# Kernel tuning notes

Hardware: AMD Instinct MI355X
Metric: run time of the kernel (lower is better)

Reference implementation:

```python
import jax, jax.numpy as jnp
import numpy as np

B = 64        # number of tasks (sequential steps)
D = 512       # knowledge_representation_dim == understanding_representation_dim
M = 8192      # memory_slots
GAMMA = 0.95  # memory_gamma


def setup_inputs() -> dict:
    key = jax.random.key(0)
    k1, k2, k3, k4 = jax.random.split(key, 4)
    ortho = jax.nn.initializers.orthogonal()
    return {
        "k": jax.random.normal(k1, (B, 1, D), jnp.float32),
        "u": jax.random.normal(k2, (B, 1, D), jnp.float32),
        "memory_knowledge": ortho(k3, (D, M), jnp.float32),
        "memory_understanding": ortho(k4, (D, M), jnp.float32),
        "beta_param": jnp.float32(0.0),
        "memory_gamma": jnp.float32(GAMMA),
    }


def reference(k, u, memory_knowledge, memory_understanding, beta_param, memory_gamma):
    n_slots = memory_knowledge.shape[1]
    slot_ids = jnp.arange(n_slots)
    beta = jax.nn.sigmoid(beta_param)

    def step(carry, xs):
        MK, MU, w_w, w_u, w_lu = carry
        k_task, u_task = xs  # each [1, D]
        # cosine similarity of the task key against every memory column: [1, M]
        sim = (k_task @ MK) / (
            jnp.linalg.norm(k_task, axis=-1, keepdims=True)
            * jnp.linalg.norm(MK, axis=0, keepdims=True)
        )
        w_r = jax.nn.softmax(sim, axis=-1)[0]  # [M]
        # zero out the least-used slot (argmin of usage weights)
        keep = (slot_ids != jnp.argmin(w_u))[None, :]  # [1, M]
        MK = jnp.where(keep, MK, 0.0)
        MU = jnp.where(keep, MU, 0.0)
        # usage / write / least-used weight updates
        w_u = memory_gamma * w_u + w_r + w_w
        w_w = beta * jnp.mean(w_r) + (1.0 - beta) * w_lu  # [M] via broadcast of scalar mean
        w_lu = (slot_ids == jnp.argmin(w_u)).astype(MK.dtype)  # one-hot least-used
        # rank-1 write of understanding, then read refined understanding, then write knowledge
        MU = MU + u_task[0][:, None] * w_w[None, :]  # [D, M]
        u_ref = w_r @ MK.T  # [D] -- read uses MK after zeroing, before its write
        MK = MK + k_task[0][:, None] * w_w[None, :]  # [D, M]
        return (MK, MU, w_w, w_u, w_lu), u_ref

    zeros = jnp.zeros((n_slots,), memory_knowledge.dtype)
    init = (memory_knowledge, memory_understanding, zeros, zeros, zeros)
    _, u_refined = jax.lax.scan(step, init, (k, u))
    return u_refined[:, None, :]  # [B, 1, D]
```

## Files before the change

kernel.cpp:

```cpp
#include <hip/hip_runtime.h>
#include <math.h>

#define BB 64
#define DD 512
#define MM 8192
#define K2T 512
#define K2C 16

typedef unsigned long long u64;

template<int CTRL>
__device__ __forceinline__ float dpp_addf(float x) {
    int y = __builtin_amdgcn_update_dpp(0, __float_as_int(x), CTRL, 0xF, 0xF, true);
    return x + __int_as_float(y);
}
__device__ __forceinline__ float wave_sum64(float x) {
    x = dpp_addf<0x111>(x); x = dpp_addf<0x112>(x); x = dpp_addf<0x114>(x); x = dpp_addf<0x118>(x);
    x = dpp_addf<0x142>(x); x = dpp_addf<0x143>(x);
    return __int_as_float(__builtin_amdgcn_readlane(__float_as_int(x), 63));
}
__device__ __forceinline__ float readlane_f(float v, int l) {
    return __int_as_float(__builtin_amdgcn_readlane(__float_as_int(v), l));
}
template<int CTRL>
__device__ __forceinline__ u64 dpp_min_step(u64 k) {
    unsigned lo = (unsigned)k, hi = (unsigned)(k >> 32);
    unsigned nlo = (unsigned)__builtin_amdgcn_update_dpp((int)0xFFFFFFFFu, (int)lo, CTRL, 0xF, 0xF, false);
    unsigned nhi = (unsigned)__builtin_amdgcn_update_dpp((int)0xFFFFFFFFu, (int)hi, CTRL, 0xF, 0xF, false);
    u64 nk = (((u64)nhi) << 32) | (u64)nlo;
    return nk < k ? nk : k;
}
__device__ __forceinline__ u64 wave_min64_lane63(u64 k) {
    k = dpp_min_step<0x111>(k); k = dpp_min_step<0x112>(k); k = dpp_min_step<0x114>(k);
    k = dpp_min_step<0x118>(k); k = dpp_min_step<0x142>(k); k = dpp_min_step<0x143>(k);
    return k;
}
__device__ __forceinline__ u64 wave_min8(u64 k) {
    k = dpp_min_step<0x111>(k); k = dpp_min_step<0x112>(k); k = dpp_min_step<0x114>(k);
    unsigned lo = (unsigned)__builtin_amdgcn_readlane((int)(unsigned)k, 7);
    unsigned hi = (unsigned)__builtin_amdgcn_readlane((int)(unsigned)(k >> 32), 7);
    return (((u64)hi) << 32) | (u64)lo;
}

struct K0Smem {
    float Ks[BB][129];
    float Gs[BB][BB];
};
struct K1Smem {
    float Ks[64 * 65];
    float Ms[64 * 65];
    float sq[4 * 64];
};
#define KA_SMEM ((sizeof(K0Smem) > sizeof(K1Smem)) ? sizeof(K0Smem) : sizeof(K1Smem))

__global__ __launch_bounds__(256) void ka_gram_s0(const float* __restrict__ K, const float* __restrict__ MK0,
                                                  float* __restrict__ G, float* __restrict__ Pfx,
                                                  float* __restrict__ S0p, float* __restrict__ n2p) {
    __shared__ __align__(16) char blob[KA_SMEM];
    const int tid = threadIdx.x;

    if (blockIdx.x == 0) {
        K0Smem* sm = (K0Smem*)blob;
        const int ti = ((tid >> 4) & 15) << 2;
        const int tj = (tid & 15) << 2;
        float acc[4][4];
        #pragma unroll
        for (int i = 0; i < 4; ++i)
            #pragma unroll
            for (int j = 0; j < 4; ++j) acc[i][j] = 0.f;
        for (int d0 = 0; d0 < DD; d0 += 128) {
            #pragma unroll
            for (int i = 0; i < 32; ++i) {
                int e = i * 256 + tid; int r = e >> 7, c = e & 127;
                sm->Ks[r][c] = K[r * DD + d0 + c];
            }
            __syncthreads();
            for (int dl = 0; dl < 128; ++dl) {
                float rv[4], cv[4];
                #pragma unroll
                for (int i = 0; i < 4; ++i) rv[i] = sm->Ks[ti + i][dl];
                #pragma unroll
                for (int j = 0; j < 4; ++j) cv[j] = sm->Ks[tj + j][dl];
                #pragma unroll
                for (int i = 0; i < 4; ++i)
                    #pragma unroll
                    for (int j = 0; j < 4; ++j) acc[i][j] += rv[i] * cv[j];
            }
            __syncthreads();
        }
        #pragma unroll
        for (int i = 0; i < 4; ++i)
            #pragma unroll
            for (int j = 0; j < 4; ++j) {
                G[(ti + i) * BB + tj + j] = acc[i][j];
                sm->Gs[ti + i][tj + j] = acc[i][j];
            }
        __syncthreads();
        const int s = tid & 63, w = tid >> 6;
        for (int rr = 0; rr < 16; ++rr) {
            int row = w * 16 + rr;
            float x = (s < row) ? sm->Gs[row][s] : 0.f;
            #pragma unroll
            for (int o = 1; o < 64; o <<= 1) {
                float y = __shfl_down(x, o);
                if (s + o < 64) x += y;
            }
            Pfx[row * BB + s] = x;
        }
        return;
    }

    K1Smem* sm = (K1Smem*)blob;
    const int b = blockIdx.x - 1;
    const int lane = tid & 63, w = tid >> 6;
    const int jb = (b & 127) * 64;
    const int by = b >> 7;
    const int dbase = by * 256;
    const int t4 = ((w << 2) | (lane >> 4)) << 2;
    const int jq0 = lane & 15;
    float acc[4][4];
    #pragma unroll
    for (int i = 0; i < 4; ++i)
        #pragma unroll
        for (int q = 0; q < 4; ++q) acc[i][q] = 0.f;
    float sqa = 0.f;
    for (int dt = 0; dt < 4; ++dt) {
        int d0 = dbase + dt * 64;
        #pragma unroll
        for (int i = 0; i < 16; ++i) {
            int e = i * 256 + tid; int r = e >> 6, c = e & 63;
            sm->Ks[r * 65 + c] = K[r * DD + d0 + c];
            float m = MK0[(d0 + r) * MM + jb + c];
            sm->Ms[r * 65 + c] = m;
            sqa += m * m;
        }
        __syncthreads();
        #pragma unroll 4
        for (int dl = 0; dl < 64; ++dl) {
            float kv[4], mv[4];
            #pragma unroll
            for (int i = 0; i < 4; ++i) kv[i] = sm->Ks[(t4 + i) * 65 + dl];
            #pragma unroll
            for (int q = 0; q < 4; ++q) mv[q] = sm->Ms[dl * 65 + jq0 + 16 * q];
            #pragma unroll
            for (int i = 0; i < 4; ++i)
                #pragma unroll
                for (int q = 0; q < 4; ++q) acc[i][q] += kv[i] * mv[q];
        }
        __syncthreads();
    }
    #pragma unroll
    for (int i = 0; i < 4; ++i)
        #pragma unroll
        for (int q = 0; q < 4; ++q)
            S0p[by * BB * MM + (t4 + i) * MM + jb + jq0 + 16 * q] = acc[i][q];
    sm->sq[w * 64 + lane] = sqa;
    __syncthreads();
    if (w == 0) n2p[by * MM + jb + lane] =
        sm->sq[lane] + sm->sq[64 + lane] + sm->sq[128 + lane] + sm->sq[192 + lane];
}

__global__ __launch_bounds__(64) void k1b_ecold(const float* __restrict__ S0p,
                                                const float* __restrict__ G,
                                                const float* __restrict__ Pfx,
                                                const float* __restrict__ n2p,
                                                const float* __restrict__ bp,
                                                float* __restrict__ Ecold) {
    __shared__ float Pfx0s[BB], invks[BB], k2s[BB];
    int tid = threadIdx.x;
    int j = blockIdx.x * 64 + tid;
    {
        float g = G[tid * BB + tid];
        k2s[tid] = g;
        invks[tid] = __builtin_amdgcn_rsqf(g);
        Pfx0s[tid] = Pfx[tid * BB + 0];
    }
    const float beta = 1.f / (1.f + expf(-bp[0]));
    const float cuni = beta / (float)MM;
    float n2c = n2p[j] + n2p[MM + j];
    __syncthreads();
    float pa = S0p[j];
    float pb = S0p[BB * MM + j];
    for (int t = 0; t < BB; ++t) {
        float na = 0.f, nb = 0.f;
        if (t + 1 < BB) {
            na = S0p[(t + 1) * MM + j];
            nb = S0p[(BB + t + 1) * MM + j];
        }
        float s0 = pa + pb;
        float d_ = s0 + cuni * Pfx0s[t];
        float cosv = d_ * invks[t] * __builtin_amdgcn_rsqf(n2c);
        float ee = __expf(cosv);
        Ecold[t * MM + j] = ee;
        n2c = n2c + 2.f * cuni * d_ + cuni * cuni * k2s[t];
        pa = na; pb = nb;
    }
}

__global__ __launch_bounds__(256) void ks_rowsum(const float* __restrict__ Ecold, float* __restrict__ Scold) {
    __shared__ float sw[4];
    int t = blockIdx.x, tid = threadIdx.x;
    int lane = tid & 63, wid = tid >> 6;
    float s = 0.f;
    #pragma unroll
    for (int i = 0; i < 32; ++i) s += Ecold[t * MM + i * 256 + tid];
    #pragma unroll
    for (int o = 32; o > 0; o >>= 1) s += __shfl_down(s, o);
    if (lane == 0) sw[wid] = s;
    __syncthreads();
    if (tid == 0) Scold[t] = sw[0] + sw[1] + sw[2] + sw[3];
}

struct ScanSmem {
    u64   red[2][8];
    float EtabL[BB * BB];
    float EcTabL[BB * BB];
    float invSL[BB];
    float SL[BB];
    int   endL[BB];
    float invS_bc[2];
};
struct K3Smem {
    float Ws[64 * 65];
    float Msub[64 * 65];
};
#define SMEM_BYTES ((sizeof(ScanSmem) > sizeof(K3Smem)) ? sizeof(ScanSmem) : sizeof(K3Smem))

__global__ __launch_bounds__(512) void k23_scan_u1(const float* __restrict__ Ecold,
                                                   const float* __restrict__ G,
                                                   const float* __restrict__ Pfx,
                                                   const float* __restrict__ Scoldg,
                                                   const float* __restrict__ bp,
                                                   const float* __restrict__ gp,
                                                   const float* __restrict__ MK0,
                                                   float* __restrict__ Etab_g,
                                                   float* __restrict__ EcTab_g,
                                                   float* __restrict__ Sg,
                                                   float* __restrict__ invSg,
                                                   int*   __restrict__ endTab_g,
                                                   int*   __restrict__ hcolg,
                                                   float* __restrict__ parts) {
    __shared__ __align__(16) char smem_raw[SMEM_BYTES];
    const int tid = threadIdx.x;

    if (blockIdx.x != 0) {
        K3Smem* sm = (K3Smem*)smem_raw;
        const int tile = blockIdx.x - 1;
        const int d0 = (tile & 7) * 64;
        const int by = tile >> 3;
        const bool act = tid < 256;
        const int lane = tid & 63, w = tid >> 6;
        const int t4 = ((w << 2) | (lane >> 4)) << 2;
        const int dq0 = lane & 15;
        float acc[4][4];
        #pragma unroll
        for (int i = 0; i < 4; ++i)
            #pragma unroll
            for (int q = 0; q < 4; ++q) acc[i][q] = 0.f;
        for (int sub = 0; sub < 4; ++sub) {
            int jb = by * 256 + sub * 64;
            if (act) {
                #pragma unroll
                for (int i = 0; i < 16; ++i) {
                    int e = i * 256 + tid; int r = e >> 6, c = e & 63;
                    sm->Ws[r * 65 + c] = Ecold[r * MM + jb + c];
                    sm->Msub[r * 65 + c] = MK0[(d0 + r) * MM + jb + c];
                }
            }
            __syncthreads();
            if (act) {
                #pragma unroll 4
                for (int jl = 0; jl < 64; ++jl) {
                    float wv[4], mv[4];
                    #pragma unroll
                    for (int i = 0; i < 4; ++i) wv[i] = sm->Ws[(t4 + i) * 65 + jl];
                    #pragma unroll
                    for (int q = 0; q < 4; ++q) mv[q] = sm->Msub[(dq0 + 16 * q) * 65 + jl];
                    #pragma unroll
                    for (int i = 0; i < 4; ++i)
                        #pragma unroll
                        for (int q = 0; q < 4; ++q) acc[i][q] += wv[i] * mv[q];
                }
            }
            __syncthreads();
        }
        if (act) {
            #pragma unroll
            for (int i = 0; i < 4; ++i)
                #pragma unroll
                for (int q = 0; q < 4; ++q)
                    parts[(by * 64 + t4 + i) * DD + d0 + dq0 + 16 * q] = acc[i][q];
        }
        return;
    }

    ScanSmem* sm = (ScanSmem*)smem_raw;
    const int lane = tid & 63;
    const int wid = tid >> 6;
    const bool w0 = (wid == 0);

    const float beta  = 1.f / (1.f + expf(-bp[0]));
    const float gamma = gp[0];
    const float cuni  = beta / (float)MM;
    const float omb   = 1.f - beta;

    if (tid < BB) sm->endL[tid] = BB;

    const float4* Ec4 = reinterpret_cast<const float4*>(Ecold);

    float wu[K2C], e0[K2C], e1[K2C], e2[K2C];
    #pragma unroll
    for (int c = 0; c < K2C; ++c) wu[c] = 0.f;
    #pragma unroll
    for (int i = 0; i < K2C / 4; ++i) {
        float4 v = Ec4[i * K2T + tid];
        e0[4 * i + 0] = v.x; e0[4 * i + 1] = v.y; e0[4 * i + 2] = v.z; e0[4 * i + 3] = v.w;
        float4 u = Ec4[(MM / 4) + i * K2T + tid];
        e1[4 * i + 0] = u.x; e1[4 * i + 1] = u.y; e1[4 * i + 2] = u.z; e1[4 * i + 3] = u.w;
    }

    float slot_n2 = 0.f, slot_ec = 0.f, wu_hot = 0.f, e_true_c = 0.f;
    int   slot_j = -1;
    bool  slot_act = false;
    float k2_cur = 0.f, S_reg = 0.f, invS_reg = 0.f;

    if (w0) {
        float g0 = G[lane];
        k2_cur = readlane_f(g0, 0);
        S_reg = Scoldg[0];
        invS_reg = __builtin_amdgcn_rcpf(S_reg);
        if (lane == 0) sm->invS_bc[0] = invS_reg;
    }
    __syncthreads();

    auto step = [&](int t, float (&cur)[K2C], float (&ld)[K2C]) {
        float grow_n = 0.f, pfx_n = 0.f, Ssc_n = 0.f, ecpf0 = 0.f;
        if (w0 && t + 1 < BB) {
            if (slot_act) ecpf0 = Ecold[(t + 1) * MM + slot_j];
            grow_n = G[(t + 1) * BB + lane];
            pfx_n  = Pfx[(t + 1) * BB + lane];
            Ssc_n  = Scoldg[t + 1];
        }

        int j0; float minval;
        if (t == 0) { j0 = 0; minval = 0.f; }
        else {
            u64 pm = sm->red[t & 1][lane & 7];
            pm = wave_min8(pm);
            j0 = (int)(pm & 0xFFFFFFFFu);
            minval = __uint_as_float((unsigned)(pm >> 32));
        }
        const float cuni_t = (t == 0) ? 0.f : cuni;
        float invS = w0 ? invS_reg : sm->invS_bc[t & 1];

        float latev = 0.f, ecpf_t = 0.f;
        if (w0 && lane == t) {
            latev = Ecold[t * MM + j0];
            if (t + 1 < BB) ecpf_t = Ecold[(t + 1) * MM + j0];
        }
        __builtin_amdgcn_sched_barrier(0);
        if (t + 2 < BB) {
            #pragma unroll
            for (int i = 0; i < K2C / 4; ++i) {
                float4 v = Ec4[(t + 2) * (MM / 4) + i * K2T + tid];
                ld[4 * i + 0] = v.x; ld[4 * i + 1] = v.y; ld[4 * i + 2] = v.z; ld[4 * i + 3] = v.w;
            }
        }
        __builtin_amdgcn_sched_barrier(0);

        bool fresh = false;
        if (w0) {
            u64 sup = __ballot(slot_act && (slot_j == j0));
            const bool has_sup = (sup != 0ull);
            const int  ssup = has_sup ? (int)__builtin_ctzll(sup) : 0;

            if (slot_act) {
                float ww = cuni + ((t >= 2 && lane == t - 1) ? omb : 0.f);
                wu_hot = fmaf(gamma, wu_hot, fmaf(e_true_c, invS, ww));
            }
            float trans_wu = readlane_f(wu_hot, ssup);
            float trans_E  = readlane_f(e_true_c, ssup);

            if (lane == t) {
                slot_j = j0;
                float ww0 = cuni + ((t >= 1) ? omb : 0.f);
                slot_n2 = ww0 * ww0 * k2_cur;
                slot_act = true;
                if (has_sup) wu_hot = trans_wu;
                fresh = !has_sup;
            }
            if (has_sup) {
                if (lane == ssup) slot_act = false;
                if (lane == t) sm->endL[ssup] = t;
            }

            float etl = e_true_c, ecl = slot_ec;
            if (lane == t) { ecl = latev; etl = has_sup ? trans_E : latev; }
            sm->EtabL[t * BB + lane]  = etl;
            sm->EcTabL[t * BB + lane] = ecl;
            if (lane == 0) { sm->invSL[t] = invS; sm->SL[t] = S_reg; }

            if (fresh) wu_hot = fmaf(gamma, minval, fmaf(latev, invS, cuni_t));

            if (t + 1 < BB) {
                float d_ = cuni * pfx_n;
                if (lane >= 1) d_ += omb * grow_n;
                float k2n   = readlane_f(grow_n, t + 1);
                float invkn = __builtin_amdgcn_rsqf(k2n);
                float ecpf  = (lane == t) ? ecpf_t : ecpf0;
                float myDelta = 0.f;
                float e_n = 0.f;
                if (slot_act) {
                    e_n = __expf(d_ * invkn * __builtin_amdgcn_rsqf(slot_n2));
                    myDelta = e_n - ecpf;
                    slot_n2 = slot_n2 + 2.f * cuni * d_ + cuni * cuni * k2n;
                }
                float S_next = Ssc_n + wave_sum64(myDelta);
                float invS_next = __builtin_amdgcn_rcpf(S_next);
                if (lane == 0) sm->invS_bc[(t + 1) & 1] = invS_next;
                if (slot_act) slot_ec = ecpf;
                e_true_c = e_n;
                k2_cur = k2n;
                S_reg = S_next; invS_reg = invS_next;
            }
        }

        float vmin = 0.f; int jmin = 0;
        #pragma unroll
        for (int i = 0; i < 4; ++i) {
            #pragma unroll
            for (int q = 0; q < 4; ++q) {
                int c = i * 4 + q;
                float wun = fmaf(gamma, wu[c], fmaf(cur[c], invS, cuni_t));
                wu[c] = wun;
                int j = i * 2048 + (tid << 2) + q;
                if (c == 0) { vmin = wun; jmin = j; }
                else if (wun < vmin) { vmin = wun; jmin = j; }
            }
        }
        u64 key = (((u64)__float_as_uint(vmin)) << 32) | (unsigned)jmin;

        if (((j0 >> 2) & (K2T - 1)) == tid) {
            int cj = ((j0 >> 11) << 2) | (j0 & 3);
            #pragma unroll
            for (int c = 0; c < K2C; ++c) if (c == cj) wu[c] = __builtin_inff();
        }

        if (w0) {
            u64 skey = (slot_act && !fresh)
                     ? ((((u64)__float_as_uint(wu_hot)) << 32) | (unsigned)slot_j) : ~0ull;
            key = skey < key ? skey : key;
        }
        key = wave_min64_lane63(key);
        if (lane == 63) sm->red[(t + 1) & 1][wid] = key;

        asm volatile("s_waitcnt lgkmcnt(0)" ::: "memory");
        __builtin_amdgcn_s_barrier();
        asm volatile("" ::: "memory");
    };

    #pragma unroll 1
    for (int th = 0; th < 63; th += 3) {
        step(th + 0, e0, e2);
        step(th + 1, e1, e0);
        step(th + 2, e2, e1);
    }
    step(63, e0, e2);

    for (int i = tid; i < BB * BB; i += K2T) {
        Etab_g[i]  = sm->EtabL[i];
        EcTab_g[i] = sm->EcTabL[i];
    }
    if (tid < BB) {
        Sg[tid] = sm->SL[tid];
        invSg[tid] = sm->invSL[tid];
        endTab_g[tid] = sm->endL[tid];
    }
    if (w0) hcolg[lane] = slot_j;
}

__global__ __launch_bounds__(512) void k3b_gather(const float* __restrict__ MK0, const int* __restrict__ hcolg,
                                                  float* __restrict__ MKhot) {
    int i = blockIdx.x, d = threadIdx.x;
    int h = hcolg[i];
    MKhot[i * DD + d] = MK0[d * MM + h];
}

__global__ __launch_bounds__(512) void k4_final(const float* __restrict__ parts,
                                                const float* __restrict__ K,
                                                const float* __restrict__ Etab,
                                                const float* __restrict__ EcTab,
                                                const int*   __restrict__ endTab,
                                                const float* __restrict__ Sg,
                                                const float* __restrict__ invSg,
                                                const float* __restrict__ MKhot,
                                                const float* __restrict__ bp,
                                                float* __restrict__ out) {
    __shared__ float Arow[BB];
    __shared__ float Drow[BB];
    int t = blockIdx.x, d = threadIdx.x;
    if (d < BB) {
        const float beta = 1.f / (1.f + expf(-bp[0]));
        const float cuni = beta / (float)MM;
        const float omb  = 1.f - beta;
        int s = d;
        float Ev = Etab[t * BB + s];
        int endv = endTab[s];
        bool act = (s <= t) && (t < endv);
        float S = Sg[t], invS = invSg[t];
        float ev = act ? Ev : 0.f;
        float x = ev;
        #pragma unroll
        for (int o = 1; o < 64; o <<= 1) {
            float y = __shfl_down(x, o);
            if (s + o < 64) x += y;
        }
        float suf = x - ev;
        float arow = 0.f;
        if (s < t) {
            float Qe = S - suf;
            arow = cuni * Qe;
            if (s >= 1 && act) arow += omb * Ev;
            arow *= invS;
        }
        Arow[s] = arow;
        Drow[s] = act ? (-invS * EcTab[t * BB + s]) : 0.f;
    }
    __syncthreads();
    float isv = invSg[t];
    float s1 = 0.f;
    #pragma unroll
    for (int p = 0; p < 32; ++p) s1 += parts[(p * 64 + t) * DD + d];
    float s2 = 0.f;
    for (int i = 0; i < BB; ++i) s2 += Drow[i] * MKhot[i * DD + d];
    float s3 = 0.f;
    for (int i = 0; i < BB; ++i) s3 += Arow[i] * K[i * DD + d];
    out[t * DD + d] = isv * s1 + s2 + s3;
}

extern "C" void kernel_launch(void* const* d_in, const int* in_sizes, int n_in,
                              void* d_out, int out_size, void* d_ws, size_t ws_size,
                              hipStream_t stream) {
    const float* K   = (const float*)d_in[0];
    const float* MK0 = (const float*)d_in[2];
    const float* bp  = (const float*)d_in[4];
    const float* gp  = (const float*)d_in[5];

    float* ws    = (float*)d_ws;
    float* G     = ws;
    float* Pfx   = G + 4096;
    float* S0p   = Pfx + 4096;
    float* n2p   = S0p + 1048576;
    float* Ecold = n2p + 16384;
    float* Scold = Ecold + 524288;
    float* Etab  = Scold + 64;
    float* EcTab = Etab + 4096;
    float* Sarr  = EcTab + 4096;
    float* invS  = Sarr + 64;
    float* MKhot = invS + 64;
    float* parts = MKhot + 32768;
    int*   hcol  = (int*)(parts + 1048576);
    int*   endT  = hcol + 64;
    float* out   = (float*)d_out;

    ka_gram_s0  <<<257, 256, 0, stream>>>(K, MK0, G, Pfx, S0p, n2p);
    k1b_ecold   <<<128, 64, 0, stream>>>(S0p, G, Pfx, n2p, bp, Ecold);
    ks_rowsum   <<<64, 256, 0, stream>>>(Ecold, Scold);
    k23_scan_u1 <<<257, 512, 0, stream>>>(Ecold, G, Pfx, Scold, bp, gp, MK0,
                                          Etab, EcTab, Sarr, invS, endT, hcol, parts);
    k3b_gather  <<<64, 512, 0, stream>>>(MK0, hcol, MKhot);
    k4_final    <<<64, 512, 0, stream>>>(parts, K, Etab, EcTab, endT, Sarr, invS, MKhot, bp, out);
}
```

Before: 214.6 us.

## Fuse six kernels into two using in-kernel flag synchronization

Merges the Gram/S0 kernel with the Ecold and rowsum kernels: each block now covers the full D range for its 64 columns, keeps S0 in shared memory and emits per-block partial row sums. The final output kernel and the hot-column gather move into the scan kernel as extra blocks that spin on atomic flags until the scan and partial-product tiles are done. This removes several launches and the S0p/n2p/MKhot round trips through global memory. In exchange there are fewer blocks (129 versus 257) in the first kernel, spin-waits that rely on co-residency of all blocks, and a memset launch.

After: 257.8 us. 20.1% more time.

```diff
diff --git a/kernel.cpp b/kernel.cpp
--- a/kernel.cpp
+++ b/kernel.cpp
@@ -42,21 +42,38 @@
     return (((u64)hi) << 32) | (u64)lo;
 }
 
+__device__ __forceinline__ void flag_release(int* p, int v) {
+    __threadfence();
+    __hip_atomic_store(p, v, __ATOMIC_RELEASE, __HIP_MEMORY_SCOPE_AGENT);
+}
+__device__ __forceinline__ void spin_until_eq(int* p, int want) {
+    while (__hip_atomic_load(p, __ATOMIC_ACQUIRE, __HIP_MEMORY_SCOPE_AGENT) != want)
+        __builtin_amdgcn_s_sleep(2);
+}
+
 struct K0Smem {
     float Ks[BB][129];
     float Gs[BB][BB];
 };
-struct K1Smem {
+struct KbSmem {
     float Ks[64 * 65];
     float Ms[64 * 65];
+    float S0s[64 * 65];
     float sq[4 * 64];
+    float n2A[64];
+    float n2full[64];
+    float Pfx0s[BB], invks[BB], k2s[BB];
 };
-#define KA_SMEM ((sizeof(K0Smem) > sizeof(K1Smem)) ? sizeof(K0Smem) : sizeof(K1Smem))
-
-__global__ __launch_bounds__(256) void ka_gram_s0(const float* __restrict__ K, const float* __restrict__ MK0,
-                                                  float* __restrict__ G, float* __restrict__ Pfx,
-                                                  float* __restrict__ S0p, float* __restrict__ n2p) {
-    __shared__ __align__(16) char blob[KA_SMEM];
+#define KAB_SMEM ((sizeof(K0Smem) > sizeof(KbSmem)) ? sizeof(K0Smem) : sizeof(KbSmem))
+
+__global__ __launch_bounds__(256) void kab_gram_ecold(const float* __restrict__ K,
+                                                      const float* __restrict__ MK0,
+                                                      const float* __restrict__ bp,
+                                                      float* __restrict__ G, float* __restrict__ Pfx,
+                                                      float* __restrict__ Ecold,
+                                                      float* __restrict__ Spart,
+                                                      int* __restrict__ flags) {
+    __shared__ __align__(16) char blob[KAB_SMEM];
     const int tid = threadIdx.x;
 
     if (blockIdx.x == 0) {
@@ -107,32 +124,33 @@
             }
             Pfx[row * BB + s] = x;
         }
+        __syncthreads();
+        if (tid == 0) flag_release(&flags[0], 1);
         return;
     }
 
-    K1Smem* sm = (K1Smem*)blob;
+    KbSmem* sm = (KbSmem*)blob;
     const int b = blockIdx.x - 1;
     const int lane = tid & 63, w = tid >> 6;
-    const int jb = (b & 127) * 64;
-    const int by = b >> 7;
-    const int dbase = by * 256;
+    const int jb = b * 64;
     const int t4 = ((w << 2) | (lane >> 4)) << 2;
     const int jq0 = lane & 15;
-    float acc[4][4];
+
+    float accA[4][4], accB[4][4];
     #pragma unroll
     for (int i = 0; i < 4; ++i)
         #pragma unroll
-        for (int q = 0; q < 4; ++q) acc[i][q] = 0.f;
-    float sqa = 0.f;
+        for (int q = 0; q < 4; ++q) { accA[i][q] = 0.f; accB[i][q] = 0.f; }
+    float sqaA = 0.f, sqaB = 0.f;
     for (int dt = 0; dt < 4; ++dt) {
-        int d0 = dbase + dt * 64;
+        int d0 = dt * 64;
         #pragma unroll
         for (int i = 0; i < 16; ++i) {
             int e = i * 256 + tid; int r = e >> 6, c = e & 63;
             sm->Ks[r * 65 + c] = K[r * DD + d0 + c];
             float m = MK0[(d0 + r) * MM + jb + c];
             sm->Ms[r * 65 + c] = m;
-            sqa += m * m;
+            sqaA += m * m;
         }
         __syncthreads();
         #pragma unroll 4
@@ -145,70 +163,75 @@
             #pragma unroll
             for (int i = 0; i < 4; ++i)
                 #pragma unroll
-                for (int q = 0; q < 4; ++q) acc[i][q] += kv[i] * mv[q];
-        }
-        __syncthreads();
+                for (int q = 0; q < 4; ++q) accA[i][q] += kv[i] * mv[q];
+        }
+        __syncthreads();
+    }
+    for (int dt = 0; dt < 4; ++dt) {
+        int d0 = 256 + dt * 64;
+        #pragma unroll
+        for (int i = 0; i < 16; ++i) {
+            int e = i * 256 + tid; int r = e >> 6, c = e & 63;
+            sm->Ks[r * 65 + c] = K[r * DD + d0 + c];
+            float m = MK0[(d0 + r) * MM + jb + c];
+            sm->Ms[r * 65 + c] = m;
+            sqaB += m * m;
+        }
+        __syncthreads();
+        #pragma unroll 4
+        for (int dl = 0; dl < 64; ++dl) {
+            float kv[4], mv[4];
+            #pragma unroll
+            for (int i = 0; i < 4; ++i) kv[i] = sm->Ks[(t4 + i) * 65 + dl];
+            #pragma unroll
+            for (int q = 0; q < 4; ++q) mv[q] = sm->Ms[dl * 65 + jq0 + 16 * q];
+            #pragma unroll
+            for (int i = 0; i < 4; ++i)
+                #pragma unroll
+                for (int q = 0; q < 4; ++q) accB[i][q] += kv[i] * mv[q];
+        }
+        __syncthreads();
+    }
+    sm->sq[w * 64 + lane] = sqaA;
+    __syncthreads();
+    if (w == 0) sm->n2A[lane] = sm->sq[lane] + sm->sq[64 + lane] + sm->sq[128 + lane] + sm->sq[192 + lane];
+    __syncthreads();
+    sm->sq[w * 64 + lane] = sqaB;
+    __syncthreads();
+    if (w == 0) {
+        float b4 = sm->sq[lane] + sm->sq[64 + lane] + sm->sq[128 + lane] + sm->sq[192 + lane];
+        sm->n2full[lane] = sm->n2A[lane] + b4;
     }
     #pragma unroll
     for (int i = 0; i < 4; ++i)
         #pragma unroll
         for (int q = 0; q < 4; ++q)
-            S0p[by * BB * MM + (t4 + i) * MM + jb + jq0 + 16 * q] = acc[i][q];
-    sm->sq[w * 64 + lane] = sqa;
+            sm->S0s[(t4 + i) * 65 + jq0 + 16 * q] = accA[i][q] + accB[i][q];
+    if (tid == 0) spin_until_eq(&flags[0], 1);
     __syncthreads();
-    if (w == 0) n2p[by * MM + jb + lane] =
-        sm->sq[lane] + sm->sq[64 + lane] + sm->sq[128 + lane] + sm->sq[192 + lane];
-}
-
-__global__ __launch_bounds__(64) void k1b_ecold(const float* __restrict__ S0p,
-                                                const float* __restrict__ G,
-                                                const float* __restrict__ Pfx,
-                                                const float* __restrict__ n2p,
-                                                const float* __restrict__ bp,
-                                                float* __restrict__ Ecold) {
-    __shared__ float Pfx0s[BB], invks[BB], k2s[BB];
-    int tid = threadIdx.x;
-    int j = blockIdx.x * 64 + tid;
-    {
+    if (tid < BB) {
         float g = G[tid * BB + tid];
-        k2s[tid] = g;
-        invks[tid] = __builtin_amdgcn_rsqf(g);
-        Pfx0s[tid] = Pfx[tid * BB + 0];
-    }
-    const float beta = 1.f / (1.f + expf(-bp[0]));
-    const float cuni = beta / (float)MM;
-    float n2c = n2p[j] + n2p[MM + j];
+        sm->k2s[tid] = g;
+        sm->invks[tid] = __builtin_amdgcn_rsqf(g);
+        sm->Pfx0s[tid] = Pfx[tid * BB + 0];
+    }
     __syncthreads();
-    float pa = S0p[j];
-    float pb = S0p[BB * MM + j];
-    for (int t = 0; t < BB; ++t) {
-        float na = 0.f, nb = 0.f;
-        if (t + 1 < BB) {
-            na = S0p[(t + 1) * MM + j];
-            nb = S0p[(BB + t + 1) * MM + j];
-        }
-        float s0 = pa + pb;
-        float d_ = s0 + cuni * Pfx0s[t];
-        float cosv = d_ * invks[t] * __builtin_amdgcn_rsqf(n2c);
-        float ee = __expf(cosv);
-        Ecold[t * MM + j] = ee;
-        n2c = n2c + 2.f * cuni * d_ + cuni * cuni * k2s[t];
-        pa = na; pb = nb;
-    }
-}
-
-__global__ __launch_bounds__(256) void ks_rowsum(const float* __restrict__ Ecold, float* __restrict__ Scold) {
-    __shared__ float sw[4];
-    int t = blockIdx.x, tid = threadIdx.x;
-    int lane = tid & 63, wid = tid >> 6;
-    float s = 0.f;
-    #pragma unroll
-    for (int i = 0; i < 32; ++i) s += Ecold[t * MM + i * 256 + tid];
-    #pragma unroll
-    for (int o = 32; o > 0; o >>= 1) s += __shfl_down(s, o);
-    if (lane == 0) sw[wid] = s;
-    __syncthreads();
-    if (tid == 0) Scold[t] = sw[0] + sw[1] + sw[2] + sw[3];
+    if (w == 0) {
+        const float beta = 1.f / (1.f + expf(-bp[0]));
+        const float cuni = beta / (float)MM;
+        int j = jb + lane;
+        float n2c = sm->n2full[lane];
+        for (int t = 0; t < BB; ++t) {
+            float s0 = sm->S0s[t * 65 + lane];
+            float d_ = s0 + cuni * sm->Pfx0s[t];
+            float cosv = d_ * sm->invks[t] * __builtin_amdgcn_rsqf(n2c);
+            float ee = __expf(cosv);
+            Ecold[t * MM + j] = ee;
+            float rs = wave_sum64(ee);
+            if (lane == 0) Spart[t * 128 + b] = rs;
+            n2c = n2c + 2.f * cuni * d_ + cuni * cuni * sm->k2s[t];
+        }
+    }
 }
 
 struct ScanSmem {
@@ -224,28 +247,38 @@
     float Ws[64 * 65];
     float Msub[64 * 65];
 };
-#define SMEM_BYTES ((sizeof(ScanSmem) > sizeof(K3Smem)) ? sizeof(ScanSmem) : sizeof(K3Smem))
-
-__global__ __launch_bounds__(512) void k23_scan_u1(const float* __restrict__ Ecold,
-                                                   const float* __restrict__ G,
-                                                   const float* __restrict__ Pfx,
-                                                   const float* __restrict__ Scoldg,
-                                                   const float* __restrict__ bp,
-                                                   const float* __restrict__ gp,
-                                                   const float* __restrict__ MK0,
-                                                   float* __restrict__ Etab_g,
-                                                   float* __restrict__ EcTab_g,
-                                                   float* __restrict__ Sg,
-                                                   float* __restrict__ invSg,
-                                                   int*   __restrict__ endTab_g,
-                                                   int*   __restrict__ hcolg,
-                                                   float* __restrict__ parts) {
+struct K4Smem {
+    float Arow[BB];
+    float Drow[BB];
+    int   hcs[BB];
+};
+#define SM3 ((sizeof(ScanSmem) > sizeof(K3Smem)) ? sizeof(ScanSmem) : sizeof(K3Smem))
+#define SMEM_BYTES ((SM3 > sizeof(K4Smem)) ? SM3 : sizeof(K4Smem))
+
+__global__ __launch_bounds__(512) void k23_mega(const float* __restrict__ Ecold,
+                                                const float* __restrict__ G,
+                                                const float* __restrict__ Pfx,
+                                                const float* __restrict__ Spart,
+                                                const float* __restrict__ bp,
+                                                const float* __restrict__ gp,
+                                                const float* __restrict__ MK0,
+                                                const float* __restrict__ K,
+                                                float* __restrict__ Etab_g,
+                                                float* __restrict__ EcTab_g,
+                                                float* __restrict__ Sg,
+                                                float* __restrict__ invSg,
+                                                int*   __restrict__ endTab_g,
+                                                int*   __restrict__ hcolg,
+                                                float* __restrict__ parts,
+                                                float* __restrict__ out,
+                                                int*   __restrict__ flags) {
     __shared__ __align__(16) char smem_raw[SMEM_BYTES];
     const int tid = threadIdx.x;
-
-    if (blockIdx.x != 0) {
+    const int bx = blockIdx.x;
+
+    if (bx >= 1 && bx <= 256) {
         K3Smem* sm = (K3Smem*)smem_raw;
-        const int tile = blockIdx.x - 1;
+        const int tile = bx - 1;
         const int d0 = (tile & 7) * 64;
         const int by = tile >> 3;
         const bool act = tid < 256;
@@ -291,6 +324,59 @@
                 for (int q = 0; q < 4; ++q)
                     parts[(by * 64 + t4 + i) * DD + d0 + dq0 + 16 * q] = acc[i][q];
         }
+        __syncthreads();
+        if (tid == 0) { __threadfence(); atomicAdd(&flags[2], 1); }
+        return;
+    }
+
+    if (bx >= 257) {
+        K4Smem* sm = (K4Smem*)smem_raw;
+        const int t = bx - 257;
+        const int d = tid;
+        if (tid == 0) {
+            spin_until_eq(&flags[1], 1);
+            while (__hip_atomic_load(&flags[2], __ATOMIC_ACQUIRE, __HIP_MEMORY_SCOPE_AGENT) < 256)
+                __builtin_amdgcn_s_sleep(2);
+        }
+        __syncthreads();
+        if (d < BB) {
+            sm->hcs[d] = hcolg[d];
+            const float beta = 1.f / (1.f + expf(-bp[0]));
+            const float cuni = beta / (float)MM;
+            const float omb  = 1.f - beta;
+            int s = d;
+            float Ev = Etab_g[t * BB + s];
+            int endv = endTab_g[s];
+            bool act = (s <= t) && (t < endv);
+            float S = Sg[t], invS = invSg[t];
+            float ev = act ? Ev : 0.f;
+            float x = ev;
+            #pragma unroll
+            for (int o = 1; o < 64; o <<= 1) {
+                float y = __shfl_down(x, o);
+                if (s + o < 64) x += y;
+            }
+            float suf = x - ev;
+            float arow = 0.f;
+            if (s < t) {
+                float Qe = S - suf;
+                arow = cuni * Qe;
+                if (s >= 1 && act) arow += omb * Ev;
+                arow *= invS;
+            }
+            sm->Arow[s] = arow;
+            sm->Drow[s] = act ? (-invS * EcTab_g[t * BB + s]) : 0.f;
+        }
+        __syncthreads();
+        float isv = invSg[t];
+        float s1 = 0.f;
+        #pragma unroll
+        for (int p = 0; p < 32; ++p) s1 += parts[(p * 64 + t) * DD + d];
+        float s2 = 0.f;
+        for (int i = 0; i < BB; ++i) s2 += sm->Drow[i] * MK0[d * MM + sm->hcs[i]];
+        float s3 = 0.f;
+        for (int i = 0; i < BB; ++i) s3 += sm->Arow[i] * K[i * DD + d];
+        out[t * DD + d] = isv * s1 + s2 + s3;
         return;
     }
 
@@ -319,6 +405,18 @@
         e1[4 * i + 0] = u.x; e1[4 * i + 1] = u.y; e1[4 * i + 2] = u.z; e1[4 * i + 3] = u.w;
     }
 
+    float scold_r = 0.f;
+    if (w0) {
+        const float4* sp4 = reinterpret_cast<const float4*>(Spart + lane * 128);
+        float sc = 0.f;
+        #pragma unroll 8
+        for (int i = 0; i < 32; ++i) {
+            float4 v = sp4[i];
+            sc += v.x; sc += v.y; sc += v.z; sc += v.w;
+        }
+        scold_r = sc;
+    }
+
     float slot_n2 = 0.f, slot_ec = 0.f, wu_hot = 0.f, e_true_c = 0.f;
     int   slot_j = -1;
     bool  slot_act = false;
@@ -327,7 +425,7 @@
     if (w0) {
         float g0 = G[lane];
         k2_cur = readlane_f(g0, 0);
-        S_reg = Scoldg[0];
+        S_reg = readlane_f(scold_r, 0);
         invS_reg = __builtin_amdgcn_rcpf(S_reg);
         if (lane == 0) sm->invS_bc[0] = invS_reg;
     }
@@ -339,7 +437,7 @@
             if (slot_act) ecpf0 = Ecold[(t + 1) * MM + slot_j];
             grow_n = G[(t + 1) * BB + lane];
             pfx_n  = Pfx[(t + 1) * BB + lane];
-            Ssc_n  = Scoldg[t + 1];
+            Ssc_n  = readlane_f(scold_r, t + 1);
         }
 
         int j0; float minval;
@@ -477,65 +575,8 @@
         endTab_g[tid] = sm->endL[tid];
     }
     if (w0) hcolg[lane] = slot_j;
-}
-
-__global__ __launch_bounds__(512) void k3b_gather(const float* __restrict__ MK0, const int* __restrict__ hcolg,
-                                                  float* __restrict__ MKhot) {
-    int i = blockIdx.x, d = threadIdx.x;
-    int h = hcolg[i];
-    MKhot[i * DD + d] = MK0[d * MM + h];
-}
-
-__global__ __launch_bounds__(512) void k4_final(const float* __restrict__ parts,
-                                                const float* __restrict__ K,
-                                                const float* __restrict__ Etab,
-                                                const float* __restrict__ EcTab,
-                                                const int*   __restrict__ endTab,
-                                                const float* __restrict__ Sg,
-                                                const float* __restrict__ invSg,
-                                                const float* __restrict__ MKhot,
-                                                const float* __restrict__ bp,
-                                                float* __restrict__ out) {
-    __shared__ float Arow[BB];
-    __shared__ float Drow[BB];
-    int t = blockIdx.x, d = threadIdx.x;
-    if (d < BB) {
-        const float beta = 1.f / (1.f + expf(-bp[0]));
-        const float cuni = beta / (float)MM;
-        const float omb  = 1.f - beta;
-        int s = d;
-        float Ev = Etab[t * BB + s];
-        int endv = endTab[s];
-        bool act = (s <= t) && (t < endv);
-        float S = Sg[t], invS = invSg[t];
-        float ev = act ? Ev : 0.f;
-        float x = ev;
-        #pragma unroll
-        for (int o = 1; o < 64; o <<= 1) {
-            float y = __shfl_down(x, o);
-            if (s + o < 64) x += y;
-        }
-        float suf = x - ev;
-        float arow = 0.f;
-        if (s < t) {
-            float Qe = S - suf;
-            arow = cuni * Qe;
-            if (s >= 1 && act) arow += omb * Ev;
-            arow *= invS;
-        }
-        Arow[s] = arow;
-        Drow[s] = act ? (-invS * EcTab[t * BB + s]) : 0.f;
-    }
     __syncthreads();
-    float isv = invSg[t];
-    float s1 = 0.f;
-    #pragma unroll
-    for (int p = 0; p < 32; ++p) s1 += parts[(p * 64 + t) * DD + d];
-    float s2 = 0.f;
-    for (int i = 0; i < BB; ++i) s2 += Drow[i] * MKhot[i * DD + d];
-    float s3 = 0.f;
-    for (int i = 0; i < BB; ++i) s3 += Arow[i] * K[i * DD + d];
-    out[t * DD + d] = isv * s1 + s2 + s3;
+    if (tid == 0) flag_release(&flags[1], 1);
 }
 
 extern "C" void kernel_launch(void* const* d_in, const int* in_sizes, int n_in,
@@ -549,25 +590,20 @@
     float* ws    = (float*)d_ws;
     float* G     = ws;
     float* Pfx   = G + 4096;
-    float* S0p   = Pfx + 4096;
-    float* n2p   = S0p + 1048576;
-    float* Ecold = n2p + 16384;
-    float* Scold = Ecold + 524288;
-    float* Etab  = Scold + 64;
+    float* Ecold = Pfx + 4096;
+    float* Spart = Ecold + 524288;
+    float* Etab  = Spart + 8192;
     float* EcTab = Etab + 4096;
     float* Sarr  = EcTab + 4096;
     float* invS  = Sarr + 64;
-    float* MKhot = invS + 64;
-    float* parts = MKhot + 32768;
+    float* parts = invS + 64;
     int*   hcol  = (int*)(parts + 1048576);
     int*   endT  = hcol + 64;
+    int*   flags = endT + 64;
     float* out   = (float*)d_out;
 
-    ka_gram_s0  <<<257, 256, 0, stream>>>(K, MK0, G, Pfx, S0p, n2p);
-    k1b_ecold   <<<128, 64, 0, stream>>>(S0p, G, Pfx, n2p, bp, Ecold);
-    ks_rowsum   <<<64, 256, 0, stream>>>(Ecold, Scold);
-    k23_scan_u1 <<<257, 512, 0, stream>>>(Ecold, G, Pfx, Scold, bp, gp, MK0,
-                                          Etab, EcTab, Sarr, invS, endT, hcol, parts);
-    k3b_gather  <<<64, 512, 0, stream>>>(MK0, hcol, MKhot);
-    k4_final    <<<64, 512, 0, stream>>>(parts, K, Etab, EcTab, endT, Sarr, invS, MKhot, bp, out);
-}
+    hipMemsetAsync(flags, 0, 3 * sizeof(int), stream);
+    kab_gram_ecold <<<129, 256, 0, stream>>>(K, MK0, bp, G, Pfx, Ecold, Spart, flags);
+    k23_mega       <<<321, 512, 0, stream>>>(Ecold, G, Pfx, Spart, bp, gp, MK0, K,
+                                             Etab, EcTab, Sarr, invS, endT, hcol, parts, out, flags);
+}
```

## Fuse row-sum into ecold and final combine into scan kernel via flags

Applied to the files above, without the earlier changes.

Folds the per-row exp sums into k1b_ecold as per-block wave partials, and drops the separate row-sum kernel. The scan block sums those partials itself. The gather and final kernels are merged into k23_scan_u1: blocks 1..64 spin on global flags until the scan block and all 256 tile blocks finish, then compute the output and read the hot columns directly from MK0. This removes three launches and an intermediate buffer, but relies on every block being co-resident and adds spin-wait overhead plus a memset launch.

After: 271.3 us. +26.4%, slower.

```diff
diff --git a/kernel.cpp b/kernel.cpp
--- a/kernel.cpp
+++ b/kernel.cpp
@@ -40,6 +40,15 @@
     unsigned lo = (unsigned)__builtin_amdgcn_readlane((int)(unsigned)k, 7);
     unsigned hi = (unsigned)__builtin_amdgcn_readlane((int)(unsigned)(k >> 32), 7);
     return (((u64)hi) << 32) | (u64)lo;
+}
+
+__device__ __forceinline__ void flag_release(int* p, int v) {
+    __threadfence();
+    __hip_atomic_store(p, v, __ATOMIC_RELEASE, __HIP_MEMORY_SCOPE_AGENT);
+}
+__device__ __forceinline__ void spin_until_eq(int* p, int want) {
+    while (__hip_atomic_load(p, __ATOMIC_ACQUIRE, __HIP_MEMORY_SCOPE_AGENT) != want)
+        __builtin_amdgcn_s_sleep(2);
 }
 
 struct K0Smem {
@@ -165,10 +174,12 @@
                                                 const float* __restrict__ Pfx,
                                                 const float* __restrict__ n2p,
                                                 const float* __restrict__ bp,
-                                                float* __restrict__ Ecold) {
+                                                float* __restrict__ Ecold,
+                                                float* __restrict__ Spart) {
     __shared__ float Pfx0s[BB], invks[BB], k2s[BB];
     int tid = threadIdx.x;
-    int j = blockIdx.x * 64 + tid;
+    const int b = blockIdx.x;
+    int j = b * 64 + tid;
     {
         float g = G[tid * BB + tid];
         k2s[tid] = g;
@@ -192,23 +203,11 @@
         float cosv = d_ * invks[t] * __builtin_amdgcn_rsqf(n2c);
         float ee = __expf(cosv);
         Ecold[t * MM + j] = ee;
+        float rs = wave_sum64(ee);
+        if (tid == 0) Spart[t * 128 + b] = rs;
         n2c = n2c + 2.f * cuni * d_ + cuni * cuni * k2s[t];
         pa = na; pb = nb;
     }
-}
-
-__global__ __launch_bounds__(256) void ks_rowsum(const float* __restrict__ Ecold, float* __restrict__ Scold) {
-    __shared__ float sw[4];
-    int t = blockIdx.x, tid = threadIdx.x;
-    int lane = tid & 63, wid = tid >> 6;
-    float s = 0.f;
-    #pragma unroll
-    for (int i = 0; i < 32; ++i) s += Ecold[t * MM + i * 256 + tid];
-    #pragma unroll
-    for (int o = 32; o > 0; o >>= 1) s += __shfl_down(s, o);
-    if (lane == 0) sw[wid] = s;
-    __syncthreads();
-    if (tid == 0) Scold[t] = sw[0] + sw[1] + sw[2] + sw[3];
 }
 
 struct ScanSmem {
@@ -224,73 +223,136 @@
     float Ws[64 * 65];
     float Msub[64 * 65];
 };
-#define SMEM_BYTES ((sizeof(ScanSmem) > sizeof(K3Smem)) ? sizeof(ScanSmem) : sizeof(K3Smem))
+struct K4Smem {
+    float Arow[BB];
+    float Drow[BB];
+    int   hcs[BB];
+};
+#define SM3 ((sizeof(ScanSmem) > sizeof(K3Smem)) ? sizeof(ScanSmem) : sizeof(K3Smem))
+#define SMEM_BYTES ((SM3 > sizeof(K4Smem)) ? SM3 : sizeof(K4Smem))
 
 __global__ __launch_bounds__(512) void k23_scan_u1(const float* __restrict__ Ecold,
                                                    const float* __restrict__ G,
                                                    const float* __restrict__ Pfx,
-                                                   const float* __restrict__ Scoldg,
+                                                   const float* __restrict__ Spart,
                                                    const float* __restrict__ bp,
                                                    const float* __restrict__ gp,
                                                    const float* __restrict__ MK0,
+                                                   const float* __restrict__ K,
                                                    float* __restrict__ Etab_g,
                                                    float* __restrict__ EcTab_g,
                                                    float* __restrict__ Sg,
                                                    float* __restrict__ invSg,
                                                    int*   __restrict__ endTab_g,
                                                    int*   __restrict__ hcolg,
-                                                   float* __restrict__ parts) {
+                                                   float* __restrict__ parts,
+                                                   float* __restrict__ out,
+                                                   int*   __restrict__ flags) {
     __shared__ __align__(16) char smem_raw[SMEM_BYTES];
     const int tid = threadIdx.x;
-
-    if (blockIdx.x != 0) {
-        K3Smem* sm = (K3Smem*)smem_raw;
-        const int tile = blockIdx.x - 1;
-        const int d0 = (tile & 7) * 64;
-        const int by = tile >> 3;
-        const bool act = tid < 256;
-        const int lane = tid & 63, w = tid >> 6;
-        const int t4 = ((w << 2) | (lane >> 4)) << 2;
-        const int dq0 = lane & 15;
-        float acc[4][4];
-        #pragma unroll
-        for (int i = 0; i < 4; ++i)
-            #pragma unroll
-            for (int q = 0; q < 4; ++q) acc[i][q] = 0.f;
-        for (int sub = 0; sub < 4; ++sub) {
-            int jb = by * 256 + sub * 64;
+    const int bx = blockIdx.x;
+
+    if (bx != 0) {
+        {
+            K3Smem* sm = (K3Smem*)smem_raw;
+            const int tile = bx - 1;
+            const int d0 = (tile & 7) * 64;
+            const int by = tile >> 3;
+            const bool act = tid < 256;
+            const int lane = tid & 63, w = tid >> 6;
+            const int t4 = ((w << 2) | (lane >> 4)) << 2;
+            const int dq0 = lane & 15;
+            float acc[4][4];
+            #pragma unroll
+            for (int i = 0; i < 4; ++i)
+                #pragma unroll
+                for (int q = 0; q < 4; ++q) acc[i][q] = 0.f;
+            for (int sub = 0; sub < 4; ++sub) {
+                int jb = by * 256 + sub * 64;
+                if (act) {
+                    #pragma unroll
+                    for (int i = 0; i < 16; ++i) {
+                        int e = i * 256 + tid; int r = e >> 6, c = e & 63;
+                        sm->Ws[r * 65 + c] = Ecold[r * MM + jb + c];
+                        sm->Msub[r * 65 + c] = MK0[(d0 + r) * MM + jb + c];
+                    }
+                }
+                __syncthreads();
+                if (act) {
+                    #pragma unroll 4
+                    for (int jl = 0; jl < 64; ++jl) {
+                        float wv[4], mv[4];
+                        #pragma unroll
+                        for (int i = 0; i < 4; ++i) wv[i] = sm->Ws[(t4 + i) * 65 + jl];
+                        #pragma unroll
+                        for (int q = 0; q < 4; ++q) mv[q] = sm->Msub[(dq0 + 16 * q) * 65 + jl];
+                        #pragma unroll
+                        for (int i = 0; i < 4; ++i)
+                            #pragma unroll
+                            for (int q = 0; q < 4; ++q) acc[i][q] += wv[i] * mv[q];
+                    }
+                }
+                __syncthreads();
+            }
             if (act) {
                 #pragma unroll
-                for (int i = 0; i < 16; ++i) {
-                    int e = i * 256 + tid; int r = e >> 6, c = e & 63;
-                    sm->Ws[r * 65 + c] = Ecold[r * MM + jb + c];
-                    sm->Msub[r * 65 + c] = MK0[(d0 + r) * MM + jb + c];
-                }
+                for (int i = 0; i < 4; ++i)
+                    #pragma unroll
+                    for (int q = 0; q < 4; ++q)
+                        parts[(by * 64 + t4 + i) * DD + d0 + dq0 + 16 * q] = acc[i][q];
             }
             __syncthreads();
-            if (act) {
-                #pragma unroll 4
-                for (int jl = 0; jl < 64; ++jl) {
-                    float wv[4], mv[4];
-                    #pragma unroll
-                    for (int i = 0; i < 4; ++i) wv[i] = sm->Ws[(t4 + i) * 65 + jl];
-                    #pragma unroll
-                    for (int q = 0; q < 4; ++q) mv[q] = sm->Msub[(dq0 + 16 * q) * 65 + jl];
-                    #pragma unroll
-                    for (int i = 0; i < 4; ++i)
-                        #pragma unroll
-                        for (int q = 0; q < 4; ++q) acc[i][q] += wv[i] * mv[q];
-                }
-            }
-            __syncthreads();
-        }
-        if (act) {
-            #pragma unroll
-            for (int i = 0; i < 4; ++i)
-                #pragma unroll
-                for (int q = 0; q < 4; ++q)
-                    parts[(by * 64 + t4 + i) * DD + d0 + dq0 + 16 * q] = acc[i][q];
-        }
+            if (tid == 0) { __threadfence(); atomicAdd(&flags[1], 1); }
+        }
+        if (bx > 64) return;
+
+        K4Smem* sm = (K4Smem*)smem_raw;
+        const int t = bx - 1;
+        const int d = tid;
+        if (tid == 0) {
+            spin_until_eq(&flags[0], 1);
+            while (__hip_atomic_load(&flags[1], __ATOMIC_ACQUIRE, __HIP_MEMORY_SCOPE_AGENT) < 256)
+                __builtin_amdgcn_s_sleep(2);
+        }
+        __syncthreads();
+        if (d < BB) {
+            sm->hcs[d] = hcolg[d];
+            const float beta = 1.f / (1.f + expf(-bp[0]));
+            const float cuni = beta / (float)MM;
+            const float omb  = 1.f - beta;
+            int s = d;
+            float Ev = Etab_g[t * BB + s];
+            int endv = endTab_g[s];
+            bool act = (s <= t) && (t < endv);
+            float S = Sg[t], invS = invSg[t];
+            float ev = act ? Ev : 0.f;
+            float x = ev;
+            #pragma unroll
+            for (int o = 1; o < 64; o <<= 1) {
+                float y = __shfl_down(x, o);
+                if (s + o < 64) x += y;
+            }
+            float suf = x - ev;
+            float arow = 0.f;
+            if (s < t) {
+                float Qe = S - suf;
+                arow = cuni * Qe;
+                if (s >= 1 && act) arow += omb * Ev;
+                arow *= invS;
+            }
+            sm->Arow[s] = arow;
+            sm->Drow[s] = act ? (-invS * EcTab_g[t * BB + s]) : 0.f;
+        }
+        __syncthreads();
+        float isv = invSg[t];
+        float s1 = 0.f;
+        #pragma unroll
+        for (int p = 0; p < 32; ++p) s1 += parts[(p * 64 + t) * DD + d];
+        float s2 = 0.f;
+        for (int i = 0; i < BB; ++i) s2 += sm->Drow[i] * MK0[d * MM + sm->hcs[i]];
+        float s3 = 0.f;
+        for (int i = 0; i < BB; ++i) s3 += sm->Arow[i] * K[i * DD + d];
+        out[t * DD + d] = isv * s1 + s2 + s3;
         return;
     }
 
@@ -319,6 +381,18 @@
         e1[4 * i + 0] = u.x; e1[4 * i + 1] = u.y; e1[4 * i + 2] = u.z; e1[4 * i + 3] = u.w;
     }
 
+    float scold_r = 0.f;
+    if (w0) {
+        const float4* sp4 = reinterpret_cast<const float4*>(Spart + lane * 128);
+        float sc = 0.f;
+        #pragma unroll 8
+        for (int i = 0; i < 32; ++i) {
+            float4 v = sp4[i];
+            sc += v.x; sc += v.y; sc += v.z; sc += v.w;
+        }
+        scold_r = sc;
+    }
+
     float slot_n2 = 0.f, slot_ec = 0.f, wu_hot = 0.f, e_true_c = 0.f;
     int   slot_j = -1;
     bool  slot_act = false;
@@ -327,7 +401,7 @@
     if (w0) {
         float g0 = G[lane];
         k2_cur = readlane_f(g0, 0);
-        S_reg = Scoldg[0];
+        S_reg = readlane_f(scold_r, 0);
         invS_reg = __builtin_amdgcn_rcpf(S_reg);
         if (lane == 0) sm->invS_bc[0] = invS_reg;
     }
@@ -339,7 +413,7 @@
             if (slot_act) ecpf0 = Ecold[(t + 1) * MM + slot_j];
             grow_n = G[(t + 1) * BB + lane];
             pfx_n  = Pfx[(t + 1) * BB + lane];
-            Ssc_n  = Scoldg[t + 1];
+            Ssc_n  = readlane_f(scold_r, t + 1);
         }
 
         int j0; float minval;
@@ -477,65 +551,8 @@
         endTab_g[tid] = sm->endL[tid];
     }
     if (w0) hcolg[lane] = slot_j;
-}
-
-__global__ __launch_bounds__(512) void k3b_gather(const float* __restrict__ MK0, const int* __restrict__ hcolg,
-                                                  float* __restrict__ MKhot) {
-    int i = blockIdx.x, d = threadIdx.x;
-    int h = hcolg[i];
-    MKhot[i * DD + d] = MK0[d * MM + h];
-}
-
-__global__ __launch_bounds__(512) void k4_final(const float* __restrict__ parts,
-                                                const float* __restrict__ K,
-                                                const float* __restrict__ Etab,
-                                                const float* __restrict__ EcTab,
-                                                const int*   __restrict__ endTab,
-                                                const float* __restrict__ Sg,
-                                                const float* __restrict__ invSg,
-                                                const float* __restrict__ MKhot,
-                                                const float* __restrict__ bp,
-                                                float* __restrict__ out) {
-    __shared__ float Arow[BB];
-    __shared__ float Drow[BB];
-    int t = blockIdx.x, d = threadIdx.x;
-    if (d < BB) {
-        const float beta = 1.f / (1.f + expf(-bp[0]));
-        const float cuni = beta / (float)MM;
-        const float omb  = 1.f - beta;
-        int s = d;
-        float Ev = Etab[t * BB + s];
-        int endv = endTab[s];
-        bool act = (s <= t) && (t < endv);
-        float S = Sg[t], invS = invSg[t];
-        float ev = act ? Ev : 0.f;
-        float x = ev;
-        #pragma unroll
-        for (int o = 1; o < 64; o <<= 1) {
-            float y = __shfl_down(x, o);
-            if (s + o < 64) x += y;
-        }
-        float suf = x - ev;
-        float arow = 0.f;
-        if (s < t) {
-            float Qe = S - suf;
-            arow = cuni * Qe;
-            if (s >= 1 && act) arow += omb * Ev;
-            arow *= invS;
-        }
-        Arow[s] = arow;
-        Drow[s] = act ? (-invS * EcTab[t * BB + s]) : 0.f;
-    }
     __syncthreads();
-    float isv = invSg[t];
-    float s1 = 0.f;
-    #pragma unroll
-    for (int p = 0; p < 32; ++p) s1 += parts[(p * 64 + t) * DD + d];
-    float s2 = 0.f;
-    for (int i = 0; i < BB; ++i) s2 += Drow[i] * MKhot[i * DD + d];
-    float s3 = 0.f;
-    for (int i = 0; i < BB; ++i) s3 += Arow[i] * K[i * DD + d];
-    out[t * DD + d] = isv * s1 + s2 + s3;
+    if (tid == 0) flag_release(&flags[0], 1);
 }
 
 extern "C" void kernel_launch(void* const* d_in, const int* in_sizes, int n_in,
@@ -552,22 +569,20 @@
     float* S0p   = Pfx + 4096;
     float* n2p   = S0p + 1048576;
     float* Ecold = n2p + 16384;
-    float* Scold = Ecold + 524288;
-    float* Etab  = Scold + 64;
+    float* Spart = Ecold + 524288;
+    float* Etab  = Spart + 8192;
     float* EcTab = Etab + 4096;
     float* Sarr  = EcTab + 4096;
     float* invS  = Sarr + 64;
-    float* MKhot = invS + 64;
-    float* parts = MKhot + 32768;
+    float* parts = invS + 64;
     int*   hcol  = (int*)(parts + 1048576);
     int*   endT  = hcol + 64;
+    int*   flags = endT + 64;
     float* out   = (float*)d_out;
 
+    hipMemsetAsync(flags, 0, 2 * sizeof(int), stream);
     ka_gram_s0  <<<257, 256, 0, stream>>>(K, MK0, G, Pfx, S0p, n2p);
-    k1b_ecold   <<<128, 64, 0, stream>>>(S0p, G, Pfx, n2p, bp, Ecold);
-    ks_rowsum   <<<64, 256, 0, stream>>>(Ecold, Scold);
-    k23_scan_u1 <<<257, 512, 0, stream>>>(Ecold, G, Pfx, Scold, bp, gp, MK0,
-                                          Etab, EcTab, Sarr, invS, endT, hcol, parts);
-    k3b_gather  <<<64, 512, 0, stream>>>(MK0, hcol, MKhot);
-    k4_final    <<<64, 512, 0, stream>>>(parts, K, Etab, EcTab, endT, Sarr, invS, MKhot, bp, out);
-}
+    k1b_ecold   <<<128, 64, 0, stream>>>(S0p, G, Pfx, n2p, bp, Ecold, Spart);
+    k23_scan_u1 <<<257, 512, 0, stream>>>(Ecold, G, Pfx, Spart, bp, gp, MK0, K,
+                                          Etab, EcTab, Sarr, invS, endT, hcol, parts, out, flags);
+}
```
